# Optimization experiments

Hardware: AMD Instinct MI355X
Metric: run time of the kernel (lower is better)

The kernel has to match this reference:

```python
import jax, jax.numpy as jnp
import numpy as np

N_NODES = 50000
N_EDGES = 800000
DIM = 64


def _param(key, shape, scale):
    return jax.random.normal(key, shape, dtype=jnp.float32) * scale


def setup_inputs() -> dict:
    key = jax.random.key(0)
    ks = jax.random.split(key, 20)
    s = 1.0 / np.sqrt(DIM)
    x = jax.random.normal(ks[0], (N_NODES, DIM), dtype=jnp.float32)
    weights = jax.random.uniform(ks[1], (6,), dtype=jnp.float32)
    edge_index = jax.random.randint(ks[2], (2, N_EDGES), 0, N_NODES, dtype=jnp.int64)
    return {
        "x": x,
        "weights": weights,
        # mlp
        "W_mlp": _param(ks[3], (DIM, DIM), s), "b_mlp": jnp.zeros((DIM,), jnp.float32),
        # sage (mean aggregator): lin_l on neighbor mean, lin_r on self
        "Wl_sage": _param(ks[4], (DIM, DIM), s), "Wr_sage": _param(ks[5], (DIM, DIM), s),
        "b_sage": jnp.zeros((DIM,), jnp.float32),
        # gcn
        "W_gcn": _param(ks[6], (DIM, DIM), s), "b_gcn": jnp.zeros((DIM,), jnp.float32),
        # gat (single head)
        "W_gat": _param(ks[7], (DIM, DIM), s),
        "a_src": _param(ks[8], (DIM,), s), "a_dst": _param(ks[9], (DIM,), s),
        "b_gat": jnp.zeros((DIM,), jnp.float32),
        # chebconv K=3
        "W_cheb": _param(ks[10], (3, DIM, DIM), s), "b_cheb": jnp.zeros((DIM,), jnp.float32),
        # gin (eps=0, nn = Linear)
        "W_gin": _param(ks[11], (DIM, DIM), s), "b_gin": jnp.zeros((DIM,), jnp.float32),
        "edge_index": edge_index,
    }


def _mixed_forward(x, weights, W_mlp, b_mlp, Wl_sage, Wr_sage, b_sage,
                   W_gcn, b_gcn, W_gat, a_src, a_dst, b_gat,
                   W_cheb, b_cheb, W_gin, b_gin, edge_index):
    N = x.shape[0]
    src, dst = edge_index[0], edge_index[1]
    seg_sum = lambda v, idx: jax.ops.segment_sum(v, idx, num_segments=N)

    deg = seg_sum(jnp.ones(src.shape[0], x.dtype), dst)  # in-degree [N]
    nsum = seg_sum(x[src], dst)                           # sum of neighbor feats [N, D]

    # --- mlp (graph-free) ---
    o_mlp = x @ W_mlp + b_mlp

    # --- sage, mean aggregation ---
    nmean = nsum / jnp.maximum(deg, 1.0)[:, None]
    o_sage = nmean @ Wl_sage + x @ Wr_sage + b_sage

    # --- gcn with self loops: D'^{-1/2} (A+I) D'^{-1/2} X W ---
    dinv = jax.lax.rsqrt(deg + 1.0)
    xw = x @ W_gcn
    norm_e = dinv[src] * dinv[dst]
    o_gcn = seg_sum(norm_e[:, None] * xw[src], dst) + xw * (dinv * dinv)[:, None] + b_gcn

    # --- gat, single head, self loops appended, leaky_relu(0.2) scoring ---
    h = x @ W_gat
    el, er = h @ a_src, h @ a_dst
    loop = jnp.arange(N, dtype=src.dtype)
    src2 = jnp.concatenate([src, loop])
    dst2 = jnp.concatenate([dst, loop])
    e = jax.nn.leaky_relu(el[src2] + er[dst2], 0.2)
    m = jax.ops.segment_max(e, dst2, num_segments=N)
    p = jnp.exp(e - m[dst2])
    z = jax.ops.segment_sum(p, dst2, num_segments=N)
    alpha = p / (z[dst2] + 1e-16)
    o_gat = jax.ops.segment_sum(alpha[:, None] * h[src2], dst2, num_segments=N) + b_gat

    # --- cheb K=3, lambda_max=2: L_hat = L_norm - I = -A_norm ---
    dinv_c = jax.lax.rsqrt(jnp.maximum(deg, 1.0))
    nrm = dinv_c[src] * dinv_c[dst]
    prop = lambda t: seg_sum(nrm[:, None] * t[src], dst)
    T0 = x
    T1 = -prop(T0)
    T2 = -2.0 * prop(T1) - T0
    o_cheb = T0 @ W_cheb[0] + T1 @ W_cheb[1] + T2 @ W_cheb[2] + b_cheb

    # --- gin, eps=0, nn = Linear ---
    o_gin = (x + nsum) @ W_gin + b_gin

    outs = (o_mlp, o_sage, o_gcn, o_gat, o_cheb, o_gin)
    res = jnp.zeros_like(o_mlp)
    for k, o in enumerate(outs):
        res = res + weights[k] * jax.nn.elu(o)
    return res


def reference(x, weights, W_mlp, b_mlp, Wl_sage, Wr_sage, b_sage,
              W_gcn, b_gcn, W_gat, a_src, a_dst, b_gat,
              W_cheb, b_cheb, W_gin, b_gin, edge_index):
    return _mixed_forward(x, weights, W_mlp, b_mlp, Wl_sage, Wr_sage, b_sage,
                          W_gcn, b_gcn, W_gat, a_src, a_dst, b_gat,
                          W_cheb, b_cheb, W_gin, b_gin, edge_index)
```

## Files before the change

### kernel.cpp

```cpp
#include <hip/hip_runtime.h>
#include <cstdint>
#include <cstddef>

#define NN 50000
#define NE 800000
#define CAP 96
#define NSEG 8
#define SEGW 6250

constexpr size_t O_CNT   = 0;
constexpr size_t O_SLOT  = 50048;
constexpr size_t O_NODAL = O_SLOT + (size_t)NN*CAP;
constexpr size_t O_VA    = O_NODAL + 200000;
constexpr size_t O_VB    = O_VA + 64;
constexpr size_t O_XB    = O_VB + 64;
constexpr size_t O_NSB   = O_XB + 1600032;
constexpr size_t O_T1B   = O_NSB + 1600000;
constexpr size_t O_V1B   = O_T1B + 1600032;
constexpr size_t O_GB    = O_V1B + 1600000;
constexpr size_t O_UB    = O_GB  + 1600000;
constexpr size_t O_WPK   = O_UB  + 1600000;

typedef __attribute__((ext_vector_type(8))) short short8;
typedef __attribute__((ext_vector_type(4))) float f32x4;

__device__ __forceinline__ float leaky02(float v){ return v >= 0.f ? v : 0.2f*v; }
__device__ __forceinline__ float eluf(float v){ return v > 0.f ? v : (__expf(v) - 1.f); }

__device__ __forceinline__ void lds_fence(){
  asm volatile("s_waitcnt lgkmcnt(0)" ::: "memory");
}

__device__ __forceinline__ unsigned short f2bf(float f){
  unsigned u = __float_as_uint(f);
  unsigned r = (u + 0x7FFFu + ((u >> 16) & 1u)) >> 16;
  return (unsigned short)r;
}
__device__ __forceinline__ float bf2f(unsigned short b){
  return __uint_as_float(((unsigned)b) << 16);
}
__device__ __forceinline__ unsigned pack2(unsigned short lo, unsigned short hi){
  return (unsigned)lo | ((unsigned)hi << 16);
}

__global__ __launch_bounds__(256) void k_scatter(
    const int* __restrict__ src, const int* __restrict__ dst,
    int* __restrict__ cnt, unsigned short* __restrict__ slot,
    const float* __restrict__ W_mlp, const float* __restrict__ Wr,
    const float* __restrict__ W_cheb, const float* __restrict__ W_gin,
    const float* __restrict__ Wl, const float* __restrict__ W_gcn,
    const float* __restrict__ W_gat,
    const float* __restrict__ a_src, const float* __restrict__ a_dst,
    const float4* __restrict__ x4,
    float* __restrict__ va, float* __restrict__ vb,
    unsigned short* __restrict__ wpk,
    ushort4* __restrict__ xb4, ushort4* __restrict__ t1b4){
  int b = blockIdx.x;
  int seg = b & (NSEG-1);
  int lo = seg * SEGW;
  int e = (b >> 3)*256 + threadIdx.x;
  if (e < NE){
    int d = dst[e];
    if ((unsigned)(d - lo) < (unsigned)SEGW){
      int s = src[e];
      int pos = atomicAdd(&cnt[d], 1);
      if (pos < CAP) slot[(size_t)d*CAP + pos] = (unsigned short)s;
    }
  }
  if (b == 0){
    int k = threadIdx.x;
    if (k < 64){
      float sa = 0.f, sb = 0.f;
      for (int j = 0; j < 64; ++j){
        float w = W_gat[k*64 + j];
        sa = fmaf(w, a_src[j], sa);
        sb = fmaf(w, a_dst[j], sb);
      }
      va[k] = sa; vb[k] = sb;
    }
  } else if (b <= 9){
    int w = b - 1;
    const float* s; const float* sub = nullptr;
    switch (w){
      case 0: s = W_mlp; break;
      case 1: s = Wr; break;
      case 2: s = W_cheb; sub = W_cheb + 8192; break;
      case 3: s = W_gin; break;
      case 4: s = Wl; break;
      case 5: s = W_cheb + 4096; break;
      case 6: s = W_cheb + 8192; break;
      case 7: s = W_gcn; break;
      default: s = W_gat; break;
    }
    for (int ee = threadIdx.x; ee < 4096; ee += 256){
      int k = ee >> 6, n = ee & 63;
      float f = s[ee];
      if (sub) f -= sub[ee];
      wpk[(size_t)w*4096 + (size_t)n*64 + k] = f2bf(f);
    }
  } else if (b < 3136){
    int i = (b - 10)*256 + threadIdx.x;
    if (i < NN*16){
      float4 v = x4[i];
      ushort4 o;
      o.x = f2bf(v.x); o.y = f2bf(v.y); o.z = f2bf(v.z); o.w = f2bf(v.w);
      xb4[i] = o;
    } else if (i < (NN+1)*16){
      ushort4 z; z.x = 0; z.y = 0; z.z = 0; z.w = 0;
      xb4[i] = z;
      t1b4[i] = z;
    }
  }
}

__global__ __launch_bounds__(256) void k_nodal(const unsigned short* __restrict__ xb,
    const int* __restrict__ cnt, const float* __restrict__ va, const float* __restrict__ vb,
    float4* __restrict__ nodal){
  int tid = threadIdx.x;
  int li = tid & 15;
  int row = blockIdx.x*16 + (tid >> 4);
  if (row >= NN) return;
  ushort4 hb = *(const ushort4*)&xb[(size_t)row*64 + li*4];
  float4 hv = make_float4(bf2f(hb.x), bf2f(hb.y), bf2f(hb.z), bf2f(hb.w));
  float4 av = *(const float4*)&va[li*4];
  float4 bv = *(const float4*)&vb[li*4];
  float ps = hv.x*av.x + hv.y*av.y + hv.z*av.z + hv.w*av.w;
  float pd = hv.x*bv.x + hv.y*bv.y + hv.z*bv.z + hv.w*bv.w;
  #pragma unroll
  for (int o = 1; o < 16; o <<= 1){ ps += __shfl_xor(ps, o); pd += __shfl_xor(pd, o); }
  if (li == 0){
    float c = (float)cnt[row];
    float dinv  = rsqrtf(c + 1.f);
    float dinvc = rsqrtf(fmaxf(c, 1.f));
    nodal[row] = make_float4(dinvc, dinv, ps, pd);
  }
}

__global__ __launch_bounds__(256) void k_aggA(
    const unsigned short* __restrict__ xb,
    const int* __restrict__ cnt, const unsigned short* __restrict__ slot,
    const float4* __restrict__ nodal,
    unsigned* __restrict__ nsb2, unsigned* __restrict__ t1b2,
    unsigned* __restrict__ v1b2, unsigned* __restrict__ gb2){
  __shared__ float4 sW[4][64];
  int wid  = threadIdx.x >> 6;
  int lane = threadIdx.x & 63;
  int half = lane >> 5, hl = lane & 31;
  int node = blockIdx.x*8 + wid*2 + half;
  int c = min(cnt[node], CAP);
  int cmax = max(c, __shfl_xor(c, 32));
  const unsigned short* sl = slot + (size_t)node*CAP;
  float4 nn = nodal[node];
  float ern = nn.w;
  float a0e=0.f,a0o=0.f,a1e=0.f,a1o=0.f,a2e=0.f,a2o=0.f,a3e=0.f,a3o=0.f, zl=0.f;
  for (int base = 0; base < cmax; base += 32){
    int rem = c - base;
    bool act = hl < rem;
    int s = act ? (int)sl[base+hl] : NN;
    float4 ns = act ? nodal[s] : make_float4(0.f,0.f,0.f,0.f);
    float p = act ? __expf(fminf(leaky02(ns.z + ern), 60.f)) : 0.f;
    zl += p;
    sW[wid][lane] = make_float4(__int_as_float(s), ns.x, ns.y, p);
    lds_fence();
    int remw = min(32, cmax - base);
    for (int j = 0; j < remw; j += 8){
      float4 w[8]; unsigned uv[8];
      #pragma unroll
      for (int q2 = 0; q2 < 8; ++q2){
        w[q2] = sW[wid][half*32 + j + q2];
        int sb = __float_as_int(w[q2].x);
        sb = ((unsigned)sb <= (unsigned)NN) ? sb : NN;
        uv[q2] = *(const unsigned*)&xb[(size_t)sb*64 + 2*hl];
      }
      #pragma unroll
      for (int q2 = 0; q2 < 8; ++q2){
        float lo = __uint_as_float(uv[q2] << 16);
        float hi = __uint_as_float(uv[q2] & 0xffff0000u);
        a0e += lo;                       a0o += hi;
        a1e = fmaf(w[q2].y, lo, a1e);    a1o = fmaf(w[q2].y, hi, a1o);
        a2e = fmaf(w[q2].z, lo, a2e);    a2o = fmaf(w[q2].z, hi, a2o);
        a3e = fmaf(w[q2].w, lo, a3e);    a3o = fmaf(w[q2].w, hi, a3o);
      }
    }
    lds_fence();
  }
  #pragma unroll
  for (int o = 1; o <= 16; o <<= 1) zl += __shfl_xor(zl, o);
  unsigned uxs = *(const unsigned*)&xb[(size_t)node*64 + 2*hl];
  float xsx = __uint_as_float(uxs << 16);
  float xsy = __uint_as_float(uxs & 0xffff0000u);
  float p_self = __expf(fminf(leaky02(nn.z + nn.w), 60.f));
  float rz = 1.f / (zl + p_self + 1e-16f);
  size_t off2 = (size_t)node*32 + hl;
  nsb2[off2] = pack2(f2bf(a0e), f2bf(a0o));
  t1b2[off2] = pack2(f2bf(-nn.x*a1e), f2bf(-nn.x*a1o));
  v1b2[off2] = pack2(f2bf(nn.y*a2e + nn.y*nn.y*xsx), f2bf(nn.y*a2o + nn.y*nn.y*xsy));
  gb2[off2]  = pack2(f2bf((a3e + p_self*xsx)*rz), f2bf((a3o + p_self*xsy)*rz));
}

__global__ __launch_bounds__(256) void k_aggB(const unsigned short* __restrict__ t1b,
    const int* __restrict__ cnt, const unsigned short* __restrict__ slot,
    const float4* __restrict__ nodal, unsigned* __restrict__ ub2){
  __shared__ float2 sW[4][64];
  int wid  = threadIdx.x >> 6;
  int lane = threadIdx.x & 63;
  int half = lane >> 5, hl = lane & 31;
  int node = blockIdx.x*8 + wid*2 + half;
  int c = min(cnt[node], CAP);
  int cmax = max(c, __shfl_xor(c, 32));
  const unsigned short* sl = slot + (size_t)node*CAP;
  const float* nf = (const float*)nodal;
  float ae = 0.f, ao = 0.f;
  for (int base = 0; base < cmax; base += 32){
    int rem = c - base;
    bool act = hl < rem;
    int s = act ? (int)sl[base+hl] : NN;
    float dc = act ? nf[(size_t)s*4] : 0.f;
    sW[wid][lane] = make_float2(__int_as_float(s), dc);
    lds_fence();
    int remw = min(32, cmax - base);
    for (int j = 0; j < remw; j += 8){
      float2 w[8]; unsigned uv[8];
      #pragma unroll
      for (int q2 = 0; q2 < 8; ++q2){
        w[q2] = sW[wid][half*32 + j + q2];
        int sb = __float_as_int(w[q2].x);
        sb = ((unsigned)sb <= (unsigned)NN) ? sb : NN;
        uv[q2] = *(const unsigned*)&t1b[(size_t)sb*64 + 2*hl];
      }
      #pragma unroll
      for (int q2 = 0; q2 < 8; ++q2){
        float lo = __uint_as_float(uv[q2] << 16);
        float hi = __uint_as_float(uv[q2] & 0xffff0000u);
        ae = fmaf(w[q2].y, lo, ae);
        ao = fmaf(w[q2].y, hi, ao);
      }
    }
    lds_fence();
  }
  float sc = -2.f * nodal[node].x;
  ub2[(size_t)node*32 + hl] = pack2(f2bf(sc*ae), f2bf(sc*ao));
}

__global__ __launch_bounds__(64) void k_epi(
    const float* __restrict__ wts,
    const float* __restrict__ b_mlp, const float* __restrict__ b_sage,
    const float* __restrict__ b_gcn, const float* __restrict__ b_gat,
    const float* __restrict__ b_cheb, const float* __restrict__ b_gin,
    const float4* __restrict__ nodal, const unsigned short* __restrict__ wpk,
    const unsigned short* __restrict__ xb, const unsigned short* __restrict__ nsb,
    const unsigned short* __restrict__ t1b, const unsigned short* __restrict__ v1b,
    const unsigned short* __restrict__ gb, const unsigned short* __restrict__ ub,
    float* __restrict__ out){
  const int lane = threadIdx.x;
  const int ml   = lane & 15;
  const int q    = lane >> 4;
  const int rowbase = blockIdx.x*16;
  const float w0 = wts[0], w1 = wts[1], w2 = wts[2], w3 = wts[3], w4 = wts[4], w5 = wts[5];
  const float* nod = (const float*)nodal;

  short8 ah0, ah1;

  auto loadA = [&](const unsigned short* __restrict__ src){
    const unsigned short* p = src + (size_t)(rowbase + ml)*64 + q*8;
    ah0 = *(const short8*)p;
    ah1 = *(const short8*)(p + 32);
  };
  auto group = [&](int w, f32x4 acc[4]){
    const unsigned short* base = wpk + (size_t)w*4096;
    #pragma unroll
    for (int nt = 0; nt < 4; ++nt){
      const unsigned short* bp = base + (size_t)(nt*16 + ml)*64;
      short8 b0 = *(const short8*)(bp + q*8);
      short8 b1 = *(const short8*)(bp + 32 + q*8);
      acc[nt] = __builtin_amdgcn_mfma_f32_16x16x32_bf16(ah0, b0, acc[nt], 0, 0, 0);
      acc[nt] = __builtin_amdgcn_mfma_f32_16x16x32_bf16(ah1, b1, acc[nt], 0, 0, 0);
    }
  };

  f32x4 res[4];
  #pragma unroll
  for (int i = 0; i < 4; ++i) res[i] = (f32x4){0.f,0.f,0.f,0.f};

  auto emit = [&](const f32x4 acc[4], const float* __restrict__ bias, float wk){
    #pragma unroll
    for (int nt = 0; nt < 4; ++nt){
      float b = bias[nt*16 + ml];
      #pragma unroll
      for (int r = 0; r < 4; ++r) res[nt][r] += wk * eluf(acc[nt][r] + b);
    }
  };

  f32x4 t[4], accC[4], accWr[4], accG[4];

  loadA(v1b);
  #pragma unroll
  for (int i=0;i<4;++i) t[i] = (f32x4){0.f,0.f,0.f,0.f};
  group(7, t); emit(t, b_gcn, w2);
  loadA(gb);
  #pragma unroll
  for (int i=0;i<4;++i) t[i] = (f32x4){0.f,0.f,0.f,0.f};
  group(8, t); emit(t, b_gat, w3);
  loadA(ub);
  #pragma unroll
  for (int i=0;i<4;++i) accC[i] = (f32x4){0.f,0.f,0.f,0.f};
  group(6, accC);
  loadA(t1b);
  group(5, accC);
  loadA(xb);
  #pragma unroll
  for (int i=0;i<4;++i) t[i] = (f32x4){0.f,0.f,0.f,0.f};
  group(0, t); emit(t, b_mlp, w0);
  #pragma unroll
  for (int i=0;i<4;++i) accWr[i] = (f32x4){0.f,0.f,0.f,0.f};
  group(1, accWr);
  group(2, accC); emit(accC, b_cheb, w4);
  #pragma unroll
  for (int i=0;i<4;++i) accG[i] = (f32x4){0.f,0.f,0.f,0.f};
  group(3, accG);
  loadA(nsb);
  group(3, accG); emit(accG, b_gin, w5);
  #pragma unroll
  for (int i=0;i<4;++i) t[i] = (f32x4){0.f,0.f,0.f,0.f};
  group(4, t);
  #pragma unroll
  for (int nt = 0; nt < 4; ++nt){
    float b = b_sage[nt*16 + ml];
    #pragma unroll
    for (int r = 0; r < 4; ++r){
      int row = rowbase + q*4 + r;
      float dc = nod[(size_t)row*4];
      float invd = dc*dc;
      res[nt][r] += w1 * eluf(invd*t[nt][r] + accWr[nt][r] + b);
    }
  }
  #pragma unroll
  for (int nt = 0; nt < 4; ++nt){
    int col = nt*16 + ml;
    #pragma unroll
    for (int r = 0; r < 4; ++r){
      int row = rowbase + q*4 + r;
      out[(size_t)row*64 + col] = res[nt][r];
    }
  }
}

extern "C" void kernel_launch(void* const* d_in, const int* in_sizes, int n_in,
                              void* d_out, int out_size, void* d_ws, size_t ws_size,
                              hipStream_t stream){
  const float* x      = (const float*)d_in[0];
  const float* wts    = (const float*)d_in[1];
  const float* W_mlp  = (const float*)d_in[2];
  const float* b_mlp  = (const float*)d_in[3];
  const float* Wl     = (const float*)d_in[4];
  const float* Wr     = (const float*)d_in[5];
  const float* b_sage = (const float*)d_in[6];
  const float* W_gcn  = (const float*)d_in[7];
  const float* b_gcn  = (const float*)d_in[8];
  const float* W_gat  = (const float*)d_in[9];
  const float* a_src  = (const float*)d_in[10];
  const float* a_dst  = (const float*)d_in[11];
  const float* b_gat  = (const float*)d_in[12];
  const float* W_cheb = (const float*)d_in[13];
  const float* b_cheb = (const float*)d_in[14];
  const float* W_gin  = (const float*)d_in[15];
  const float* b_gin  = (const float*)d_in[16];
  const int*   ei     = (const int*)d_in[17];

  float* wsf  = (float*)d_ws;
  int*  cnt   = (int*)d_ws;
  unsigned short* slot = (unsigned short*)(wsf + O_SLOT);
  float4* nodal = (float4*)(wsf + O_NODAL);
  float* va   = wsf + O_VA;
  float* vb   = wsf + O_VB;
  unsigned short* xbu = (unsigned short*)(wsf + O_XB);
  unsigned short* nsb = (unsigned short*)(wsf + O_NSB);
  unsigned short* t1b = (unsigned short*)(wsf + O_T1B);
  unsigned short* v1b = (unsigned short*)(wsf + O_V1B);
  unsigned short* gb  = (unsigned short*)(wsf + O_GB);
  unsigned short* ub  = (unsigned short*)(wsf + O_UB);
  unsigned short* wpk = (unsigned short*)(wsf + O_WPK);
  float* out  = (float*)d_out;

  hipMemsetAsync(cnt, 0, NN*sizeof(int), stream);
  k_scatter <<<25000,256, 0, stream>>>(ei, ei + NE, cnt, slot,
                                       W_mlp, Wr, W_cheb, W_gin, Wl, W_gcn, W_gat,
                                       a_src, a_dst, (const float4*)x,
                                       va, vb, wpk, (ushort4*)xbu, (ushort4*)t1b);
  k_nodal   <<<3125, 256, 0, stream>>>(xbu, cnt, va, vb, nodal);
  k_aggA    <<<6250, 256, 0, stream>>>(xbu, cnt, slot, nodal,
                                       (unsigned*)nsb, (unsigned*)t1b,
                                       (unsigned*)v1b, (unsigned*)gb);
  k_aggB    <<<6250, 256, 0, stream>>>(t1b, cnt, slot, nodal, (unsigned*)ub);
  k_epi     <<<3125,  64, 0, stream>>>(wts, b_mlp, b_sage, b_gcn, b_gat, b_cheb, b_gin,
                                       nodal, wpk, xbu, nsb, t1b, v1b, gb, ub, out);
}
```

Measured before the change: 219.0 us.

## Fuse second Chebyshev propagation into epilogue kernel, dropping k_aggB

```diff
diff --git a/kernel.cpp b/kernel.cpp
--- a/kernel.cpp
+++ b/kernel.cpp
@@ -18,8 +18,7 @@
 constexpr size_t O_T1B   = O_NSB + 1600000;
 constexpr size_t O_V1B   = O_T1B + 1600032;
 constexpr size_t O_GB    = O_V1B + 1600000;
-constexpr size_t O_UB    = O_GB  + 1600000;
-constexpr size_t O_WPK   = O_UB  + 1600000;
+constexpr size_t O_WPK   = O_GB  + 1600000;
 
 typedef __attribute__((ext_vector_type(8))) short short8;
 typedef __attribute__((ext_vector_type(4))) float f32x4;
@@ -198,50 +197,6 @@
   gb2[off2]  = pack2(f2bf((a3e + p_self*xsx)*rz), f2bf((a3o + p_self*xsy)*rz));
 }
 
-__global__ __launch_bounds__(256) void k_aggB(const unsigned short* __restrict__ t1b,
-    const int* __restrict__ cnt, const unsigned short* __restrict__ slot,
-    const float4* __restrict__ nodal, unsigned* __restrict__ ub2){
-  __shared__ float2 sW[4][64];
-  int wid  = threadIdx.x >> 6;
-  int lane = threadIdx.x & 63;
-  int half = lane >> 5, hl = lane & 31;
-  int node = blockIdx.x*8 + wid*2 + half;
-  int c = min(cnt[node], CAP);
-  int cmax = max(c, __shfl_xor(c, 32));
-  const unsigned short* sl = slot + (size_t)node*CAP;
-  const float* nf = (const float*)nodal;
-  float ae = 0.f, ao = 0.f;
-  for (int base = 0; base < cmax; base += 32){
-    int rem = c - base;
-    bool act = hl < rem;
-    int s = act ? (int)sl[base+hl] : NN;
-    float dc = act ? nf[(size_t)s*4] : 0.f;
-    sW[wid][lane] = make_float2(__int_as_float(s), dc);
-    lds_fence();
-    int remw = min(32, cmax - base);
-    for (int j = 0; j < remw; j += 8){
-      float2 w[8]; unsigned uv[8];
-      #pragma unroll
-      for (int q2 = 0; q2 < 8; ++q2){
-        w[q2] = sW[wid][half*32 + j + q2];
-        int sb = __float_as_int(w[q2].x);
-        sb = ((unsigned)sb <= (unsigned)NN) ? sb : NN;
-        uv[q2] = *(const unsigned*)&t1b[(size_t)sb*64 + 2*hl];
-      }
-      #pragma unroll
-      for (int q2 = 0; q2 < 8; ++q2){
-        float lo = __uint_as_float(uv[q2] << 16);
-        float hi = __uint_as_float(uv[q2] & 0xffff0000u);
-        ae = fmaf(w[q2].y, lo, ae);
-        ao = fmaf(w[q2].y, hi, ao);
-      }
-    }
-    lds_fence();
-  }
-  float sc = -2.f * nodal[node].x;
-  ub2[(size_t)node*32 + hl] = pack2(f2bf(sc*ae), f2bf(sc*ao));
-}
-
 __global__ __launch_bounds__(64) void k_epi(
     const float* __restrict__ wts,
     const float* __restrict__ b_mlp, const float* __restrict__ b_sage,
@@ -250,7 +205,8 @@
     const float4* __restrict__ nodal, const unsigned short* __restrict__ wpk,
     const unsigned short* __restrict__ xb, const unsigned short* __restrict__ nsb,
     const unsigned short* __restrict__ t1b, const unsigned short* __restrict__ v1b,
-    const unsigned short* __restrict__ gb, const unsigned short* __restrict__ ub,
+    const unsigned short* __restrict__ gb,
+    const int* __restrict__ cnt, const unsigned short* __restrict__ slot,
     float* __restrict__ out){
   const int lane = threadIdx.x;
   const int ml   = lane & 15;
@@ -278,6 +234,50 @@
     }
   };
 
+  f32x4 t[4], accC[4], accWr[4], accG[4];
+
+  {
+    const int node = rowbase + ml;
+    const int c = min(cnt[node], CAP);
+    const unsigned short* sl = slot + (size_t)node*CAP;
+    const float* nf = (const float*)nodal;
+    float ac[16];
+    #pragma unroll
+    for (int i = 0; i < 16; ++i) ac[i] = 0.f;
+    for (int i = 0; i < c; i += 4){
+      float dcv[4]; short8 u0[4], u1[4];
+      #pragma unroll
+      for (int k = 0; k < 4; ++k){
+        bool act = (i + k) < c;
+        int s = act ? (int)sl[i + k] : NN;
+        dcv[k] = act ? nf[(size_t)s*4] : 0.f;
+        const unsigned short* p = t1b + (size_t)s*64 + q*8;
+        u0[k] = *(const short8*)p;
+        u1[k] = *(const short8*)(p + 32);
+      }
+      #pragma unroll
+      for (int k = 0; k < 4; ++k){
+        float dc = dcv[k];
+        #pragma unroll
+        for (int j = 0; j < 8; ++j){
+          ac[j]     = fmaf(dc, bf2f((unsigned short)u0[k][j]), ac[j]);
+          ac[8 + j] = fmaf(dc, bf2f((unsigned short)u1[k][j]), ac[8 + j]);
+        }
+      }
+    }
+    const float sc = -2.f * nodal[node].x;
+    short8 a0, a1;
+    #pragma unroll
+    for (int j = 0; j < 8; ++j){
+      a0[j] = (short)f2bf(sc * ac[j]);
+      a1[j] = (short)f2bf(sc * ac[8 + j]);
+    }
+    ah0 = a0; ah1 = a1;
+  }
+  #pragma unroll
+  for (int i=0;i<4;++i) accC[i] = (f32x4){0.f,0.f,0.f,0.f};
+  group(6, accC);
+
   f32x4 res[4];
   #pragma unroll
   for (int i = 0; i < 4; ++i) res[i] = (f32x4){0.f,0.f,0.f,0.f};
@@ -290,8 +290,6 @@
       for (int r = 0; r < 4; ++r) res[nt][r] += wk * eluf(acc[nt][r] + b);
     }
   };
-
-  f32x4 t[4], accC[4], accWr[4], accG[4];
 
   loadA(v1b);
   #pragma unroll
@@ -301,10 +299,6 @@
   #pragma unroll
   for (int i=0;i<4;++i) t[i] = (f32x4){0.f,0.f,0.f,0.f};
   group(8, t); emit(t, b_gat, w3);
-  loadA(ub);
-  #pragma unroll
-  for (int i=0;i<4;++i) accC[i] = (f32x4){0.f,0.f,0.f,0.f};
-  group(6, accC);
   loadA(t1b);
   group(5, accC);
   loadA(xb);
@@ -378,7 +372,6 @@
   unsigned short* t1b = (unsigned short*)(wsf + O_T1B);
   unsigned short* v1b = (unsigned short*)(wsf + O_V1B);
   unsigned short* gb  = (unsigned short*)(wsf + O_GB);
-  unsigned short* ub  = (unsigned short*)(wsf + O_UB);
   unsigned short* wpk = (unsigned short*)(wsf + O_WPK);
   float* out  = (float*)d_out;
 
@@ -391,7 +384,7 @@
   k_aggA    <<<6250, 256, 0, stream>>>(xbu, cnt, slot, nodal,
                                        (unsigned*)nsb, (unsigned*)t1b,
                                        (unsigned*)v1b, (unsigned*)gb);
-  k_aggB    <<<6250, 256, 0, stream>>>(t1b, cnt, slot, nodal, (unsigned*)ub);
   k_epi     <<<3125,  64, 0, stream>>>(wts, b_mlp, b_sage, b_gcn, b_gat, b_cheb, b_gin,
-                                       nodal, wpk, xbu, nsb, t1b, v1b, gb, ub, out);
-}
+                                       nodal, wpk, xbu, nsb, t1b, v1b, gb,
+                                       cnt, slot, out);
+}
```

New measurement: 225.5 us. 3.0% more time.

## Interleave node segments across blocks and split epilogue columns across four waves

Applied to the files above, without the earlier changes.

```diff
diff --git a/kernel.cpp b/kernel.cpp
--- a/kernel.cpp
+++ b/kernel.cpp
@@ -146,8 +146,13 @@
   int wid  = threadIdx.x >> 6;
   int lane = threadIdx.x & 63;
   int half = lane >> 5, hl = lane & 31;
-  int node = blockIdx.x*8 + wid*2 + half;
-  int c = min(cnt[node], CAP);
+  int b    = blockIdx.x;
+  int seg  = b & (NSEG-1);
+  int idx  = b >> 3;
+  int lbase = idx*8 + wid*2 + half;
+  bool vld = lbase < SEGW;
+  int node = seg*SEGW + (vld ? lbase : 0);
+  int c = vld ? min(cnt[node], CAP) : 0;
   int cmax = max(c, __shfl_xor(c, 32));
   const unsigned short* sl = slot + (size_t)node*CAP;
   float4 nn = nodal[node];
@@ -191,11 +196,13 @@
   float xsy = __uint_as_float(uxs & 0xffff0000u);
   float p_self = __expf(fminf(leaky02(nn.z + nn.w), 60.f));
   float rz = 1.f / (zl + p_self + 1e-16f);
-  size_t off2 = (size_t)node*32 + hl;
-  nsb2[off2] = pack2(f2bf(a0e), f2bf(a0o));
-  t1b2[off2] = pack2(f2bf(-nn.x*a1e), f2bf(-nn.x*a1o));
-  v1b2[off2] = pack2(f2bf(nn.y*a2e + nn.y*nn.y*xsx), f2bf(nn.y*a2o + nn.y*nn.y*xsy));
-  gb2[off2]  = pack2(f2bf((a3e + p_self*xsx)*rz), f2bf((a3o + p_self*xsy)*rz));
+  if (vld){
+    size_t off2 = (size_t)node*32 + hl;
+    nsb2[off2] = pack2(f2bf(a0e), f2bf(a0o));
+    t1b2[off2] = pack2(f2bf(-nn.x*a1e), f2bf(-nn.x*a1o));
+    v1b2[off2] = pack2(f2bf(nn.y*a2e + nn.y*nn.y*xsx), f2bf(nn.y*a2o + nn.y*nn.y*xsy));
+    gb2[off2]  = pack2(f2bf((a3e + p_self*xsx)*rz), f2bf((a3o + p_self*xsy)*rz));
+  }
 }
 
 __global__ __launch_bounds__(256) void k_aggB(const unsigned short* __restrict__ t1b,
@@ -205,8 +212,13 @@
   int wid  = threadIdx.x >> 6;
   int lane = threadIdx.x & 63;
   int half = lane >> 5, hl = lane & 31;
-  int node = blockIdx.x*8 + wid*2 + half;
-  int c = min(cnt[node], CAP);
+  int b    = blockIdx.x;
+  int seg  = b & (NSEG-1);
+  int idx  = b >> 3;
+  int lbase = idx*8 + wid*2 + half;
+  bool vld = lbase < SEGW;
+  int node = seg*SEGW + (vld ? lbase : 0);
+  int c = vld ? min(cnt[node], CAP) : 0;
   int cmax = max(c, __shfl_xor(c, 32));
   const unsigned short* sl = slot + (size_t)node*CAP;
   const float* nf = (const float*)nodal;
@@ -238,11 +250,13 @@
     }
     lds_fence();
   }
-  float sc = -2.f * nodal[node].x;
-  ub2[(size_t)node*32 + hl] = pack2(f2bf(sc*ae), f2bf(sc*ao));
-}
-
-__global__ __launch_bounds__(64) void k_epi(
+  if (vld){
+    float sc = -2.f * nodal[node].x;
+    ub2[(size_t)node*32 + hl] = pack2(f2bf(sc*ae), f2bf(sc*ao));
+  }
+}
+
+__global__ __launch_bounds__(256) void k_epi2(
     const float* __restrict__ wts,
     const float* __restrict__ b_mlp, const float* __restrict__ b_sage,
     const float* __restrict__ b_gcn, const float* __restrict__ b_gat,
@@ -252,95 +266,81 @@
     const unsigned short* __restrict__ t1b, const unsigned short* __restrict__ v1b,
     const unsigned short* __restrict__ gb, const unsigned short* __restrict__ ub,
     float* __restrict__ out){
-  const int lane = threadIdx.x;
+  const int tid  = threadIdx.x;
+  const int wid  = tid >> 6;
+  const int lane = tid & 63;
   const int ml   = lane & 15;
   const int q    = lane >> 4;
-  const int rowbase = blockIdx.x*16;
+  const int b    = blockIdx.x;
+  const int seg  = b & (NSEG-1);
+  const int idx  = b >> 3;
+  const int rowbase = seg*SEGW + idx*16;
+  const int nvalid  = min(16, SEGW - idx*16);
+
+  const int ar = min(rowbase + ml, NN);
+  const size_t ro = (size_t)ar*64 + q*8;
+  short8 Au0  = *(const short8*)(ub  + ro), Au1  = *(const short8*)(ub  + ro + 32);
+  short8 Av10 = *(const short8*)(v1b + ro), Av11 = *(const short8*)(v1b + ro + 32);
+  short8 Ag0  = *(const short8*)(gb  + ro), Ag1  = *(const short8*)(gb  + ro + 32);
+  short8 At0  = *(const short8*)(t1b + ro), At1  = *(const short8*)(t1b + ro + 32);
+  short8 Ax0  = *(const short8*)(xb  + ro), Ax1  = *(const short8*)(xb  + ro + 32);
+  short8 An0  = *(const short8*)(nsb + ro), An1  = *(const short8*)(nsb + ro + 32);
+
   const float w0 = wts[0], w1 = wts[1], w2 = wts[2], w3 = wts[3], w4 = wts[4], w5 = wts[5];
   const float* nod = (const float*)nodal;
 
-  short8 ah0, ah1;
-
-  auto loadA = [&](const unsigned short* __restrict__ src){
-    const unsigned short* p = src + (size_t)(rowbase + ml)*64 + q*8;
-    ah0 = *(const short8*)p;
-    ah1 = *(const short8*)(p + 32);
+  auto groupOne = [&](int w, const short8& a0, const short8& a1, f32x4& acc){
+    const unsigned short* bp = wpk + (size_t)w*4096 + (size_t)(wid*16 + ml)*64;
+    short8 b0 = *(const short8*)(bp + q*8);
+    short8 b1 = *(const short8*)(bp + 32 + q*8);
+    acc = __builtin_amdgcn_mfma_f32_16x16x32_bf16(a0, b0, acc, 0, 0, 0);
+    acc = __builtin_amdgcn_mfma_f32_16x16x32_bf16(a1, b1, acc, 0, 0, 0);
   };
-  auto group = [&](int w, f32x4 acc[4]){
-    const unsigned short* base = wpk + (size_t)w*4096;
+
+  f32x4 res = (f32x4){0.f,0.f,0.f,0.f};
+  auto emit1 = [&](const f32x4& acc, const float* __restrict__ bias, float wk){
+    float bsv = bias[wid*16 + ml];
     #pragma unroll
-    for (int nt = 0; nt < 4; ++nt){
-      const unsigned short* bp = base + (size_t)(nt*16 + ml)*64;
-      short8 b0 = *(const short8*)(bp + q*8);
-      short8 b1 = *(const short8*)(bp + 32 + q*8);
-      acc[nt] = __builtin_amdgcn_mfma_f32_16x16x32_bf16(ah0, b0, acc[nt], 0, 0, 0);
-      acc[nt] = __builtin_amdgcn_mfma_f32_16x16x32_bf16(ah1, b1, acc[nt], 0, 0, 0);
-    }
+    for (int r = 0; r < 4; ++r) res[r] += wk * eluf(acc[r] + bsv);
   };
 
-  f32x4 res[4];
-  #pragma unroll
-  for (int i = 0; i < 4; ++i) res[i] = (f32x4){0.f,0.f,0.f,0.f};
-
-  auto emit = [&](const f32x4 acc[4], const float* __restrict__ bias, float wk){
-    #pragma unroll
-    for (int nt = 0; nt < 4; ++nt){
-      float b = bias[nt*16 + ml];
-      #pragma unroll
-      for (int r = 0; r < 4; ++r) res[nt][r] += wk * eluf(acc[nt][r] + b);
-    }
-  };
-
-  f32x4 t[4], accC[4], accWr[4], accG[4];
-
-  loadA(v1b);
-  #pragma unroll
-  for (int i=0;i<4;++i) t[i] = (f32x4){0.f,0.f,0.f,0.f};
-  group(7, t); emit(t, b_gcn, w2);
-  loadA(gb);
-  #pragma unroll
-  for (int i=0;i<4;++i) t[i] = (f32x4){0.f,0.f,0.f,0.f};
-  group(8, t); emit(t, b_gat, w3);
-  loadA(ub);
-  #pragma unroll
-  for (int i=0;i<4;++i) accC[i] = (f32x4){0.f,0.f,0.f,0.f};
-  group(6, accC);
-  loadA(t1b);
-  group(5, accC);
-  loadA(xb);
-  #pragma unroll
-  for (int i=0;i<4;++i) t[i] = (f32x4){0.f,0.f,0.f,0.f};
-  group(0, t); emit(t, b_mlp, w0);
-  #pragma unroll
-  for (int i=0;i<4;++i) accWr[i] = (f32x4){0.f,0.f,0.f,0.f};
-  group(1, accWr);
-  group(2, accC); emit(accC, b_cheb, w4);
-  #pragma unroll
-  for (int i=0;i<4;++i) accG[i] = (f32x4){0.f,0.f,0.f,0.f};
-  group(3, accG);
-  loadA(nsb);
-  group(3, accG); emit(accG, b_gin, w5);
-  #pragma unroll
-  for (int i=0;i<4;++i) t[i] = (f32x4){0.f,0.f,0.f,0.f};
-  group(4, t);
-  #pragma unroll
-  for (int nt = 0; nt < 4; ++nt){
-    float b = b_sage[nt*16 + ml];
+  f32x4 t, accC, accWr, accG;
+  accC = (f32x4){0.f,0.f,0.f,0.f};
+  groupOne(6, Au0, Au1, accC);
+  t = (f32x4){0.f,0.f,0.f,0.f};
+  groupOne(7, Av10, Av11, t); emit1(t, b_gcn, w2);
+  t = (f32x4){0.f,0.f,0.f,0.f};
+  groupOne(8, Ag0, Ag1, t); emit1(t, b_gat, w3);
+  groupOne(5, At0, At1, accC);
+  t = (f32x4){0.f,0.f,0.f,0.f};
+  groupOne(0, Ax0, Ax1, t); emit1(t, b_mlp, w0);
+  accWr = (f32x4){0.f,0.f,0.f,0.f};
+  groupOne(1, Ax0, Ax1, accWr);
+  groupOne(2, Ax0, Ax1, accC); emit1(accC, b_cheb, w4);
+  accG = (f32x4){0.f,0.f,0.f,0.f};
+  groupOne(3, Ax0, Ax1, accG);
+  groupOne(3, An0, An1, accG); emit1(accG, b_gin, w5);
+  t = (f32x4){0.f,0.f,0.f,0.f};
+  groupOne(4, An0, An1, t);
+  {
+    float bsv = b_sage[wid*16 + ml];
     #pragma unroll
     for (int r = 0; r < 4; ++r){
-      int row = rowbase + q*4 + r;
-      float dc = nod[(size_t)row*4];
-      float invd = dc*dc;
-      res[nt][r] += w1 * eluf(invd*t[nt][r] + accWr[nt][r] + b);
+      int lr = q*4 + r;
+      if (lr < nvalid){
+        int row = rowbase + lr;
+        float dc = nod[(size_t)row*4];
+        float invd = dc*dc;
+        res[r] += w1 * eluf(invd*t[r] + accWr[r] + bsv);
+      }
     }
   }
   #pragma unroll
-  for (int nt = 0; nt < 4; ++nt){
-    int col = nt*16 + ml;
-    #pragma unroll
-    for (int r = 0; r < 4; ++r){
-      int row = rowbase + q*4 + r;
-      out[(size_t)row*64 + col] = res[nt][r];
+  for (int r = 0; r < 4; ++r){
+    int lr = q*4 + r;
+    if (lr < nvalid){
+      int row = rowbase + lr;
+      out[(size_t)row*64 + wid*16 + ml] = res[r];
     }
   }
 }
@@ -388,10 +388,10 @@
                                        a_src, a_dst, (const float4*)x,
                                        va, vb, wpk, (ushort4*)xbu, (ushort4*)t1b);
   k_nodal   <<<3125, 256, 0, stream>>>(xbu, cnt, va, vb, nodal);
-  k_aggA    <<<6250, 256, 0, stream>>>(xbu, cnt, slot, nodal,
+  k_aggA    <<<6256, 256, 0, stream>>>(xbu, cnt, slot, nodal,
                                        (unsigned*)nsb, (unsigned*)t1b,
                                        (unsigned*)v1b, (unsigned*)gb);
-  k_aggB    <<<6250, 256, 0, stream>>>(t1b, cnt, slot, nodal, (unsigned*)ub);
-  k_epi     <<<3125,  64, 0, stream>>>(wts, b_mlp, b_sage, b_gcn, b_gat, b_cheb, b_gin,
+  k_aggB    <<<6256, 256, 0, stream>>>(t1b, cnt, slot, nodal, (unsigned*)ub);
+  k_epi2    <<<3128, 256, 0, stream>>>(wts, b_mlp, b_sage, b_gcn, b_gat, b_cheb, b_gin,
                                        nodal, wpk, xbu, nsb, t1b, v1b, gb, ub, out);
 }
```

After: 225.9 us. 3.1% more time.
